# Optimization experiments

Hardware: AMD Instinct MI355X
Metric: run time of the kernel (lower is better)

Reference implementation:

```python
import jax, jax.numpy as jnp
import numpy as np

B, S, D, H = 2, 2048, 1024, 16
HD = D // H  # 64

def setup_inputs() -> dict:
    key = jax.random.key(0)
    ks = jax.random.split(key, 11)
    s = 1.0 / np.sqrt(D)
    inp = {
        "q": jax.random.normal(ks[0], (B, S, D), jnp.float32),
        "k": jax.random.normal(ks[1], (B, S, D), jnp.float32),
        "v": jax.random.normal(ks[2], (B, S, D), jnp.float32),
        "Wq": jax.random.normal(ks[3], (D, D), jnp.float32) * s,
        "bq": jnp.zeros((D,), jnp.float32),
        "Wk": jax.random.normal(ks[4], (D, D), jnp.float32) * s,
        "bk": jnp.zeros((D,), jnp.float32),
        "Wv": jax.random.normal(ks[5], (D, D), jnp.float32) * s,
        "bv": jnp.zeros((D,), jnp.float32),
        "Wo": jax.random.normal(ks[6], (D, D), jnp.float32) * s,
        "bo": jnp.zeros((D,), jnp.float32),
    }
    return inp

def _split_heads(x):
    # [B,S,D] -> [B,H,S,HD]
    b = x.shape[0]
    return x.reshape(b, -1, H, HD).transpose(0, 2, 1, 3)

def reference(q, k, v, Wq, bq, Wk, bk, Wv, bv, Wo, bo):
    qh = _split_heads(q @ Wq.T + bq)
    kh = _split_heads(k @ Wk.T + bk)
    vh = _split_heads(v @ Wv.T + bv)
    scale = 1.0 / jnp.sqrt(jnp.asarray(HD, qh.dtype))
    scores = jnp.einsum("bhqd,bhkd->bhqk", qh, kh) * scale  # [B,H,S,S]
    atten = jax.nn.softmax(scores, axis=-1)  # dropout is eval-mode no-op
    ctx = jnp.einsum("bhqk,bhkd->bhqd", atten, vh)
    out = ctx.transpose(0, 2, 1, 3).reshape(q.shape[0], -1, D)
    return out @ Wo.T + bo, atten
```

## Files before the change

kernel.cpp:

```cpp
#include <hip/hip_runtime.h>
#include <cstdint>

#define B_ 2
#define S_ 2048
#define D_ 1024
#define H_ 16

typedef __bf16 bf16x8 __attribute__((ext_vector_type(8)));
typedef float  f32x4  __attribute__((ext_vector_type(4)));

__device__ __forceinline__ void g2l16(const void* g, void* l) {
  auto* gp = reinterpret_cast<const __attribute__((address_space(1))) uint32_t*>(
      reinterpret_cast<uintptr_t>(g));
  auto* lp = reinterpret_cast<__attribute__((address_space(3))) uint32_t*>(
      reinterpret_cast<uintptr_t>(l));
  __builtin_amdgcn_global_load_lds(gp, lp, 16, 0, 0);
}

__device__ __forceinline__ float exp2_hw(float x) {
#if __has_builtin(__builtin_amdgcn_exp2f)
  return __builtin_amdgcn_exp2f(x);
#else
  return __exp2f(x);
#endif
}

struct CvtArgs {
  const float* s[7];
  __bf16* d[7];
  int n[7];
};

__global__ __launch_bounds__(256) void k_cvt(CvtArgs a) {
  int t = blockIdx.y;
  long i = (long)blockIdx.x * blockDim.x + threadIdx.x;
  long base = i * 8;
  if (base >= a.n[t]) return;
  const float4* sp = (const float4*)(a.s[t] + base);
  float4 x = sp[0], y = sp[1];
  bf16x8 o;
  o[0] = (__bf16)x.x; o[1] = (__bf16)x.y; o[2] = (__bf16)x.z; o[3] = (__bf16)x.w;
  o[4] = (__bf16)y.x; o[5] = (__bf16)y.y; o[6] = (__bf16)y.z; o[7] = (__bf16)y.w;
  *(bf16x8*)(a.d[t] + base) = o;
}

__global__ __launch_bounds__(256, 3) void k_proj(
    const __bf16* __restrict__ Xq, const __bf16* __restrict__ Xk, const __bf16* __restrict__ Xv,
    const __bf16* __restrict__ Wq, const __bf16* __restrict__ Wk, const __bf16* __restrict__ Wv,
    const float* __restrict__ bq, const float* __restrict__ bk, const float* __restrict__ bv,
    __bf16* __restrict__ Oq, __bf16* __restrict__ Ok, __bf16* __restrict__ Ov)
{
  int z = blockIdx.z;
  const __bf16* X = (z == 0) ? Xq : (z == 1) ? Xk : Xv;
  const __bf16* W = (z == 0) ? Wq : (z == 1) ? Wk : Wv;
  const float* bias = (z == 0) ? bq : (z == 1) ? bk : bv;
  __bf16* O = (z == 0) ? Oq : (z == 1) ? Ok : Ov;
  float scale = (z == 0) ? 0.180336880111183f : 1.0f;

  __shared__ bf16x8 As[2][512];
  __shared__ bf16x8 Bs[2][512];

  int t = threadIdx.x, lane = t & 63, w = t >> 6;
  int l15 = lane & 15, l4 = lane >> 4;
  int wr = w >> 1, wc = w & 1;
  int m0 = blockIdx.y * 128, n0 = blockIdx.x * 128;

  int srow = t >> 2, sc = t & 3;
  int ldsoff = __builtin_amdgcn_readfirstlane(w * 1024);
  const __bf16* Xs = X + (size_t)(m0 + srow) * 1024 + sc * 8;
  const __bf16* Wsp = W + (size_t)(n0 + srow) * 1024 + sc * 8;

#define PSTAGE(buf, kt)                                                        \
  {                                                                            \
    _Pragma("unroll")                                                          \
    for (int i = 0; i < 2; ++i) {                                              \
      int lo = __builtin_amdgcn_readfirstlane(i * 4096 + ldsoff);              \
      g2l16(Xs + (size_t)i * 64 * 1024 + (kt) * 32, (char*)As[buf] + lo);      \
      g2l16(Wsp + (size_t)i * 64 * 1024 + (kt) * 32, (char*)Bs[buf] + lo);     \
    }                                                                          \
  }

  f32x4 acc[4][4] = {};

  PSTAGE(0, 0)
  asm volatile("s_waitcnt vmcnt(0)" ::: "memory");
  __builtin_amdgcn_s_barrier();
  __builtin_amdgcn_sched_barrier(0);

  for (int kt = 0; kt < 32; ++kt) {
    int cur = kt & 1;
    if (kt < 31) PSTAGE(cur ^ 1, kt + 1)

    bf16x8 af[4], bfr[4];
#pragma unroll
    for (int i = 0; i < 4; ++i) af[i] = As[cur][(wr * 64 + i * 16 + l15) * 4 + l4];
#pragma unroll
    for (int j = 0; j < 4; ++j) bfr[j] = Bs[cur][(wc * 64 + j * 16 + l15) * 4 + l4];
#pragma unroll
    for (int i = 0; i < 4; ++i)
#pragma unroll
      for (int j = 0; j < 4; ++j)
        acc[i][j] = __builtin_amdgcn_mfma_f32_16x16x32_bf16(af[i], bfr[j], acc[i][j], 0, 0, 0);

    asm volatile("s_waitcnt vmcnt(0)" ::: "memory");
    __builtin_amdgcn_s_barrier();
    __builtin_amdgcn_sched_barrier(0);
  }
#undef PSTAGE

#pragma unroll
  for (int j = 0; j < 4; ++j) {
    int col = n0 + wc * 64 + j * 16 + l15;
    float bv_ = bias[col];
    int h = col >> 6, hd = col & 63;
#pragma unroll
    for (int i = 0; i < 4; ++i) {
#pragma unroll
      for (int r = 0; r < 4; ++r) {
        int row = m0 + wr * 64 + i * 16 + l4 * 4 + r;
        int b = row >> 11, ss = row & 2047;
        float val = (acc[i][j][r] + bv_) * scale;
        O[(((size_t)b * H_ + h) * S_ + ss) * 64 + hd] = (__bf16)val;
      }
    }
  }
}

__global__ __launch_bounds__(256) void k_trans(const __bf16* __restrict__ Vh,
                                               __bf16* __restrict__ VhT)
{
  __shared__ __bf16 Tt[64][72];
  int bid = blockIdx.x;
  int bh = bid >> 5, st = bid & 31;
  int t = threadIdx.x;
  int sr = t >> 2, dc = (t & 3) * 16;
  const __bf16* src = Vh + (((size_t)bh * S_) + st * 64 + sr) * 64 + dc;
  *(bf16x8*)&Tt[sr][dc] = *(const bf16x8*)src;
  *(bf16x8*)&Tt[sr][dc + 8] = *(const bf16x8*)(src + 8);
  __syncthreads();
  int dr = t >> 2, s0 = (t & 3) * 16;
  bf16x8 o0, o1;
#pragma unroll
  for (int ii = 0; ii < 8; ++ii) { o0[ii] = Tt[s0 + ii][dr]; o1[ii] = Tt[s0 + 8 + ii][dr]; }
  __bf16* dst = VhT + ((size_t)bh * 64 + dr) * S_ + st * 64 + s0;
  *(bf16x8*)dst = o0;
  *(bf16x8*)(dst + 8) = o1;
}

__global__ __launch_bounds__(512, 4) void k_attn(
    const __bf16* __restrict__ Qh, const __bf16* __restrict__ Kh,
    const __bf16* __restrict__ VhT, float* __restrict__ atten,
    __bf16* __restrict__ ctxb)
{
  __shared__ bf16x8 Kl[2][512];
  __shared__ bf16x8 Vl[2][512];
  __shared__ bf16x8 Pl[8 * 176];

  int bid = blockIdx.x;
  int sb = (bid & 7) * 64 + (bid >> 3);
  int bh = sb >> 4, qt = sb & 15;
  int t = threadIdx.x, lane = t & 63, w = t >> 6;
  int l15 = lane & 15, l4 = lane >> 4;
  int q0 = qt * 128 + w * 16;

  const __bf16* Qp = Qh + ((size_t)bh * S_ + q0) * 64;
  bf16x8 qf0 = *(const bf16x8*)(Qp + (size_t)l15 * 64 + l4 * 8);
  bf16x8 qf1 = *(const bf16x8*)(Qp + (size_t)l15 * 64 + 32 + l4 * 8);

  int srow = t >> 3, sc8 = t & 7;
  int scs = sc8 ^ (srow & 7);
  int ldsoff = __builtin_amdgcn_readfirstlane(w * 1024);

  const __bf16* KpS = Kh + (size_t)bh * S_ * 64 + (size_t)srow * 64 + scs * 8;
  const __bf16* VpS = VhT + (size_t)bh * 64 * S_ + (size_t)srow * S_ + scs * 8;

#define QK_TILES(KBUF, SC)                                                        \
  _Pragma("unroll")                                                               \
  for (int t8 = 0; t8 < 4; ++t8) {                                                \
    int kr = t8 * 16 + l15;                                                       \
    bf16x8 kf0 = (KBUF)[kr * 8 + ((l4) ^ (kr & 7))];                              \
    bf16x8 kf1 = (KBUF)[kr * 8 + ((4 + l4) ^ (kr & 7))];                          \
    f32x4 a_ = {0.f, 0.f, 0.f, 0.f};                                              \
    a_ = __builtin_amdgcn_mfma_f32_16x16x32_bf16(qf0, kf0, a_, 0, 0, 0);          \
    a_ = __builtin_amdgcn_mfma_f32_16x16x32_bf16(qf1, kf1, a_, 0, 0, 0);          \
    SC[t8] = a_;                                                                  \
  }

  float l_part[4] = {0.f, 0.f, 0.f, 0.f};

  g2l16(KpS, (char*)Kl[0] + ldsoff);
  asm volatile("s_waitcnt vmcnt(0)" ::: "memory");
  __builtin_amdgcn_s_barrier();
  __builtin_amdgcn_sched_barrier(0);

  for (int kt = 0; kt < 32; ++kt) {
    int cur = kt & 1;
    if (kt < 31) g2l16(KpS + (size_t)(kt + 1) * 4096, (char*)Kl[cur ^ 1] + ldsoff);
    __builtin_amdgcn_sched_barrier(0);

    f32x4 sc[4];
    QK_TILES(Kl[cur], sc)

#pragma unroll
    for (int r = 0; r < 4; ++r)
      l_part[r] += (exp2_hw(sc[0][r]) + exp2_hw(sc[1][r])) +
                   (exp2_hw(sc[2][r]) + exp2_hw(sc[3][r]));

    asm volatile("s_waitcnt vmcnt(0)" ::: "memory");
    __builtin_amdgcn_s_barrier();
    __builtin_amdgcn_sched_barrier(0);
  }

  float inv_l[4];
#pragma unroll
  for (int r = 0; r < 4; ++r) {
    float l = l_part[r];
    l += __shfl_xor(l, 1);
    l += __shfl_xor(l, 2);
    l += __shfl_xor(l, 4);
    l += __shfl_xor(l, 8);
    inv_l[r] = 1.0f / l;
  }

  f32x4 ctx[4] = {};
  float* aRow = atten + ((size_t)bh * S_ + q0) * S_;
  __bf16* PlW = (__bf16*)(Pl + w * 176);

  g2l16(KpS, (char*)Kl[0] + ldsoff);
  g2l16(VpS, (char*)Vl[0] + ldsoff);
  asm volatile("s_waitcnt vmcnt(0)" ::: "memory");
  __builtin_amdgcn_s_barrier();
  __builtin_amdgcn_sched_barrier(0);

  for (int kt = 0; kt < 32; ++kt) {
    int cur = kt & 1;
    if (kt < 31) {
      g2l16(KpS + (size_t)(kt + 1) * 4096, (char*)Kl[cur ^ 1] + ldsoff);
      g2l16(VpS + (size_t)(kt + 1) * 64, (char*)Vl[cur ^ 1] + ldsoff);
    }
    __builtin_amdgcn_sched_barrier(0);

    f32x4 sc[4];
    QK_TILES(Kl[cur], sc)

#pragma unroll
    for (int t8 = 0; t8 < 4; ++t8) {
#pragma unroll
      for (int r = 0; r < 4; ++r) {
        float p = exp2_hw(sc[t8][r]) * inv_l[r];
        aRow[(size_t)(l4 * 4 + r) * S_ + kt * 64 + t8 * 16 + l15] = p;
        PlW[(l4 * 4 + r) * 88 + t8 * 16 + l15] = (__bf16)p;
      }
    }

#pragma unroll
    for (int kc = 0; kc < 2; ++kc) {
      bf16x8 pa = Pl[w * 176 + l15 * 11 + kc * 4 + l4];
#pragma unroll
      for (int dt = 0; dt < 4; ++dt) {
        int vr = dt * 16 + l15;
        bf16x8 vf = Vl[cur][vr * 8 + ((kc * 4 + l4) ^ (vr & 7))];
        ctx[dt] = __builtin_amdgcn_mfma_f32_16x16x32_bf16(pa, vf, ctx[dt], 0, 0, 0);
      }
    }

    asm volatile("s_waitcnt vmcnt(16)" ::: "memory");
    __builtin_amdgcn_s_barrier();
    __builtin_amdgcn_sched_barrier(0);
  }

  int b = bh >> 4, h = bh & 15;
#pragma unroll
  for (int dt = 0; dt < 4; ++dt) {
#pragma unroll
    for (int r = 0; r < 4; ++r) {
      size_t row = (size_t)b * S_ + q0 + l4 * 4 + r;
      ctxb[row * D_ + h * 64 + dt * 16 + l15] = (__bf16)ctx[dt][r];
    }
  }
#undef QK_TILES
}

__global__ __launch_bounds__(256, 3) void k_out(
    const __bf16* __restrict__ X, const __bf16* __restrict__ W,
    const float* __restrict__ bias, float* __restrict__ O)
{
  __shared__ bf16x8 As[2][512];
  __shared__ bf16x8 Bs[2][512];

  int t = threadIdx.x, lane = t & 63, w = t >> 6;
  int l15 = lane & 15, l4 = lane >> 4;
  int wr = w >> 1, wc = w & 1;
  int m0 = blockIdx.y * 128, n0 = blockIdx.x * 128;

  int srow = t >> 2, sc = t & 3;
  int ldsoff = __builtin_amdgcn_readfirstlane(w * 1024);
  const __bf16* Xs = X + (size_t)(m0 + srow) * 1024 + sc * 8;
  const __bf16* Wsp = W + (size_t)(n0 + srow) * 1024 + sc * 8;

#define PSTAGE(buf, kt)                                                        \
  {                                                                            \
    _Pragma("unroll")                                                          \
    for (int i = 0; i < 2; ++i) {                                              \
      int lo = __builtin_amdgcn_readfirstlane(i * 4096 + ldsoff);              \
      g2l16(Xs + (size_t)i * 64 * 1024 + (kt) * 32, (char*)As[buf] + lo);      \
      g2l16(Wsp + (size_t)i * 64 * 1024 + (kt) * 32, (char*)Bs[buf] + lo);     \
    }                                                                          \
  }

  f32x4 acc[4][4] = {};

  PSTAGE(0, 0)
  asm volatile("s_waitcnt vmcnt(0)" ::: "memory");
  __builtin_amdgcn_s_barrier();
  __builtin_amdgcn_sched_barrier(0);

  for (int kt = 0; kt < 32; ++kt) {
    int cur = kt & 1;
    if (kt < 31) PSTAGE(cur ^ 1, kt + 1)

    bf16x8 af[4], bfr[4];
#pragma unroll
    for (int i = 0; i < 4; ++i) af[i] = As[cur][(wr * 64 + i * 16 + l15) * 4 + l4];
#pragma unroll
    for (int j = 0; j < 4; ++j) bfr[j] = Bs[cur][(wc * 64 + j * 16 + l15) * 4 + l4];
#pragma unroll
    for (int i = 0; i < 4; ++i)
#pragma unroll
      for (int j = 0; j < 4; ++j)
        acc[i][j] = __builtin_amdgcn_mfma_f32_16x16x32_bf16(af[i], bfr[j], acc[i][j], 0, 0, 0);

    asm volatile("s_waitcnt vmcnt(0)" ::: "memory");
    __builtin_amdgcn_s_barrier();
    __builtin_amdgcn_sched_barrier(0);
  }
#undef PSTAGE

#pragma unroll
  for (int j = 0; j < 4; ++j) {
    int col = n0 + wc * 64 + j * 16 + l15;
    float bv_ = bias[col];
#pragma unroll
    for (int i = 0; i < 4; ++i) {
#pragma unroll
      for (int r = 0; r < 4; ++r) {
        int row = m0 + wr * 64 + i * 16 + l4 * 4 + r;
        O[(size_t)row * 1024 + col] = acc[i][j][r] + bv_;
      }
    }
  }
}

extern "C" void kernel_launch(void* const* d_in, const int* in_sizes, int n_in,
                              void* d_out, int out_size, void* d_ws, size_t ws_size,
                              hipStream_t stream)
{
  const float* q  = (const float*)d_in[0];
  const float* k  = (const float*)d_in[1];
  const float* v  = (const float*)d_in[2];
  const float* Wq = (const float*)d_in[3];
  const float* bq = (const float*)d_in[4];
  const float* Wk = (const float*)d_in[5];
  const float* bk = (const float*)d_in[6];
  const float* Wv = (const float*)d_in[7];
  const float* bv = (const float*)d_in[8];
  const float* Wo = (const float*)d_in[9];
  const float* bo = (const float*)d_in[10];

  const size_t NBSD = (size_t)B_ * S_ * D_;
  const size_t NDD  = (size_t)D_ * D_;

  float* out = (float*)d_out;
  float* atten = out + NBSD;

  if (ws_size < 2 * (NBSD * 4 + NDD * 4 + NBSD * 4)) return;

  __bf16* ws = (__bf16*)d_ws;
  __bf16* qb  = ws;
  __bf16* kb  = ws + NBSD;
  __bf16* vb  = ws + 2 * NBSD;
  __bf16* Wqb = ws + 3 * NBSD;
  __bf16* Wkb = Wqb + NDD;
  __bf16* Wvb = Wkb + NDD;
  __bf16* Wob = Wvb + NDD;
  __bf16* Qh  = Wob + NDD;
  __bf16* Kh  = Qh + NBSD;
  __bf16* Vh  = Kh + NBSD;
  __bf16* VhT = Vh + NBSD;
  __bf16* ctxb = qb;

  CvtArgs ca;
  ca.s[0] = q;  ca.d[0] = qb;  ca.n[0] = (int)NBSD;
  ca.s[1] = k;  ca.d[1] = kb;  ca.n[1] = (int)NBSD;
  ca.s[2] = v;  ca.d[2] = vb;  ca.n[2] = (int)NBSD;
  ca.s[3] = Wq; ca.d[3] = Wqb; ca.n[3] = (int)NDD;
  ca.s[4] = Wk; ca.d[4] = Wkb; ca.n[4] = (int)NDD;
  ca.s[5] = Wv; ca.d[5] = Wvb; ca.n[5] = (int)NDD;
  ca.s[6] = Wo; ca.d[6] = Wob; ca.n[6] = (int)NDD;

  k_cvt<<<dim3(2048, 7), 256, 0, stream>>>(ca);
  k_proj<<<dim3(8, 32, 3), 256, 0, stream>>>(qb, kb, vb, Wqb, Wkb, Wvb,
                                             bq, bk, bv, Qh, Kh, Vh);
  k_trans<<<dim3(1024), 256, 0, stream>>>(Vh, VhT);
  k_attn<<<dim3(512), 512, 0, stream>>>(Qh, Kh, VhT, atten, ctxb);
  k_out<<<dim3(8, 32), 256, 0, stream>>>(ctxb, Wob, bo, out);
}
```

Baseline: 264.4 us.

## Triple-buffer LDS pipelines in projection, attention and output kernels

Switches the GEMM and attention kernels from double to triple-buffered LDS rings with prefetch distance two, so waits only drain older loads (partial vmcnt) rather than all of them. The attention first pass now loads 128 keys per stage and folds exp-sum into the QK loop, and the K/V buffers are merged into one ring. Attention probabilities and output writes use nontemporal stores to cut cache pollution. This adds LDS usage, which may lower occupancy, and the hand-tuned vmcnt counts must match the number of outstanding loads.

```diff
diff --git a/kernel.cpp b/kernel.cpp
--- a/kernel.cpp
+++ b/kernel.cpp
@@ -57,8 +57,8 @@
   __bf16* O = (z == 0) ? Oq : (z == 1) ? Ok : Ov;
   float scale = (z == 0) ? 0.180336880111183f : 1.0f;
 
-  __shared__ bf16x8 As[2][512];
-  __shared__ bf16x8 Bs[2][512];
+  __shared__ bf16x8 As[3][512];
+  __shared__ bf16x8 Bs[3][512];
 
   int t = threadIdx.x, lane = t & 63, w = t >> 6;
   int l15 = lane & 15, l4 = lane >> 4;
@@ -83,13 +83,17 @@
   f32x4 acc[4][4] = {};
 
   PSTAGE(0, 0)
-  asm volatile("s_waitcnt vmcnt(0)" ::: "memory");
+  PSTAGE(1, 1)
+  asm volatile("s_waitcnt vmcnt(4)" ::: "memory");
   __builtin_amdgcn_s_barrier();
   __builtin_amdgcn_sched_barrier(0);
 
+  int ring = 0;
   for (int kt = 0; kt < 32; ++kt) {
-    int cur = kt & 1;
-    if (kt < 31) PSTAGE(cur ^ 1, kt + 1)
+    int cur = ring;
+    int rp2 = (ring == 0) ? 2 : ring - 1;
+    if (kt + 2 < 32) PSTAGE(rp2, kt + 2)
+    __builtin_amdgcn_sched_barrier(0);
 
     bf16x8 af[4], bfr[4];
 #pragma unroll
@@ -102,9 +106,16 @@
       for (int j = 0; j < 4; ++j)
         acc[i][j] = __builtin_amdgcn_mfma_f32_16x16x32_bf16(af[i], bfr[j], acc[i][j], 0, 0, 0);
 
-    asm volatile("s_waitcnt vmcnt(0)" ::: "memory");
-    __builtin_amdgcn_s_barrier();
-    __builtin_amdgcn_sched_barrier(0);
+    if (kt < 30) {
+      asm volatile("s_waitcnt vmcnt(4)" ::: "memory");
+      __builtin_amdgcn_s_barrier();
+      __builtin_amdgcn_sched_barrier(0);
+    } else if (kt == 30) {
+      asm volatile("s_waitcnt vmcnt(0)" ::: "memory");
+      __builtin_amdgcn_s_barrier();
+      __builtin_amdgcn_sched_barrier(0);
+    }
+    ring = (ring == 2) ? 0 : ring + 1;
   }
 #undef PSTAGE
 
@@ -152,8 +163,7 @@
     const __bf16* __restrict__ VhT, float* __restrict__ atten,
     __bf16* __restrict__ ctxb)
 {
-  __shared__ bf16x8 Kl[2][512];
-  __shared__ bf16x8 Vl[2][512];
+  __shared__ bf16x8 KVl[3][1024];
   __shared__ bf16x8 Pl[8 * 176];
 
   int bid = blockIdx.x;
@@ -169,47 +179,58 @@
 
   int srow = t >> 3, sc8 = t & 7;
   int scs = sc8 ^ (srow & 7);
-  int ldsoff = __builtin_amdgcn_readfirstlane(w * 1024);
+  int wbase = __builtin_amdgcn_readfirstlane(w * 1024);
 
   const __bf16* KpS = Kh + (size_t)bh * S_ * 64 + (size_t)srow * 64 + scs * 8;
   const __bf16* VpS = VhT + (size_t)bh * 64 * S_ + (size_t)srow * S_ + scs * 8;
 
-#define QK_TILES(KBUF, SC)                                                        \
-  _Pragma("unroll")                                                               \
-  for (int t8 = 0; t8 < 4; ++t8) {                                                \
-    int kr = t8 * 16 + l15;                                                       \
-    bf16x8 kf0 = (KBUF)[kr * 8 + ((l4) ^ (kr & 7))];                              \
-    bf16x8 kf1 = (KBUF)[kr * 8 + ((4 + l4) ^ (kr & 7))];                          \
-    f32x4 a_ = {0.f, 0.f, 0.f, 0.f};                                              \
-    a_ = __builtin_amdgcn_mfma_f32_16x16x32_bf16(qf0, kf0, a_, 0, 0, 0);          \
-    a_ = __builtin_amdgcn_mfma_f32_16x16x32_bf16(qf1, kf1, a_, 0, 0, 0);          \
-    SC[t8] = a_;                                                                  \
-  }
-
   float l_part[4] = {0.f, 0.f, 0.f, 0.f};
 
-  g2l16(KpS, (char*)Kl[0] + ldsoff);
-  asm volatile("s_waitcnt vmcnt(0)" ::: "memory");
+#define ASTAGE(buf, kt)                                                        \
+  {                                                                            \
+    g2l16(KpS + (size_t)(kt) * 8192, (char*)KVl[buf] + wbase);                 \
+    g2l16(KpS + (size_t)(kt) * 8192 + 4096, (char*)KVl[buf] + 8192 + wbase);   \
+  }
+
+  ASTAGE(0, 0)
+  ASTAGE(1, 1)
+  asm volatile("s_waitcnt vmcnt(2)" ::: "memory");
   __builtin_amdgcn_s_barrier();
   __builtin_amdgcn_sched_barrier(0);
 
-  for (int kt = 0; kt < 32; ++kt) {
-    int cur = kt & 1;
-    if (kt < 31) g2l16(KpS + (size_t)(kt + 1) * 4096, (char*)Kl[cur ^ 1] + ldsoff);
-    __builtin_amdgcn_sched_barrier(0);
-
-    f32x4 sc[4];
-    QK_TILES(Kl[cur], sc)
-
-#pragma unroll
-    for (int r = 0; r < 4; ++r)
-      l_part[r] += (exp2_hw(sc[0][r]) + exp2_hw(sc[1][r])) +
-                   (exp2_hw(sc[2][r]) + exp2_hw(sc[3][r]));
-
-    asm volatile("s_waitcnt vmcnt(0)" ::: "memory");
-    __builtin_amdgcn_s_barrier();
-    __builtin_amdgcn_sched_barrier(0);
-  }
+  {
+    int ring = 0;
+    for (int kt = 0; kt < 16; ++kt) {
+      int cur = ring;
+      int rp2 = (ring == 0) ? 2 : ring - 1;
+      if (kt + 2 < 16) ASTAGE(rp2, kt + 2)
+      __builtin_amdgcn_sched_barrier(0);
+
+#pragma unroll
+      for (int t8 = 0; t8 < 8; ++t8) {
+        int kr = t8 * 16 + l15;
+        bf16x8 kf0 = KVl[cur][kr * 8 + ((l4) ^ (kr & 7))];
+        bf16x8 kf1 = KVl[cur][kr * 8 + ((4 + l4) ^ (kr & 7))];
+        f32x4 a_ = {0.f, 0.f, 0.f, 0.f};
+        a_ = __builtin_amdgcn_mfma_f32_16x16x32_bf16(qf0, kf0, a_, 0, 0, 0);
+        a_ = __builtin_amdgcn_mfma_f32_16x16x32_bf16(qf1, kf1, a_, 0, 0, 0);
+#pragma unroll
+        for (int r = 0; r < 4; ++r) l_part[r] += exp2_hw(a_[r]);
+      }
+
+      if (kt < 14) {
+        asm volatile("s_waitcnt vmcnt(2)" ::: "memory");
+        __builtin_amdgcn_s_barrier();
+        __builtin_amdgcn_sched_barrier(0);
+      } else if (kt == 14) {
+        asm volatile("s_waitcnt vmcnt(0)" ::: "memory");
+        __builtin_amdgcn_s_barrier();
+        __builtin_amdgcn_sched_barrier(0);
+      }
+      ring = (ring == 2) ? 0 : ring + 1;
+    }
+  }
+#undef ASTAGE
 
   float inv_l[4];
 #pragma unroll
@@ -222,52 +243,76 @@
     inv_l[r] = 1.0f / l;
   }
 
+  __builtin_amdgcn_s_barrier();
+  __builtin_amdgcn_sched_barrier(0);
+
   f32x4 ctx[4] = {};
   float* aRow = atten + ((size_t)bh * S_ + q0) * S_;
   __bf16* PlW = (__bf16*)(Pl + w * 176);
 
-  g2l16(KpS, (char*)Kl[0] + ldsoff);
-  g2l16(VpS, (char*)Vl[0] + ldsoff);
-  asm volatile("s_waitcnt vmcnt(0)" ::: "memory");
+#define BSTAGE(buf, kt)                                                        \
+  {                                                                            \
+    g2l16(KpS + (size_t)(kt) * 4096, (char*)KVl[buf] + wbase);                 \
+    g2l16(VpS + (size_t)(kt) * 64, (char*)KVl[buf] + 8192 + wbase);            \
+  }
+
+  BSTAGE(0, 0)
+  BSTAGE(1, 1)
+  asm volatile("s_waitcnt vmcnt(2)" ::: "memory");
   __builtin_amdgcn_s_barrier();
   __builtin_amdgcn_sched_barrier(0);
 
-  for (int kt = 0; kt < 32; ++kt) {
-    int cur = kt & 1;
-    if (kt < 31) {
-      g2l16(KpS + (size_t)(kt + 1) * 4096, (char*)Kl[cur ^ 1] + ldsoff);
-      g2l16(VpS + (size_t)(kt + 1) * 64, (char*)Vl[cur ^ 1] + ldsoff);
-    }
-    __builtin_amdgcn_sched_barrier(0);
-
-    f32x4 sc[4];
-    QK_TILES(Kl[cur], sc)
-
-#pragma unroll
-    for (int t8 = 0; t8 < 4; ++t8) {
-#pragma unroll
-      for (int r = 0; r < 4; ++r) {
-        float p = exp2_hw(sc[t8][r]) * inv_l[r];
-        aRow[(size_t)(l4 * 4 + r) * S_ + kt * 64 + t8 * 16 + l15] = p;
-        PlW[(l4 * 4 + r) * 88 + t8 * 16 + l15] = (__bf16)p;
-      }
-    }
-
-#pragma unroll
-    for (int kc = 0; kc < 2; ++kc) {
-      bf16x8 pa = Pl[w * 176 + l15 * 11 + kc * 4 + l4];
-#pragma unroll
-      for (int dt = 0; dt < 4; ++dt) {
-        int vr = dt * 16 + l15;
-        bf16x8 vf = Vl[cur][vr * 8 + ((kc * 4 + l4) ^ (vr & 7))];
-        ctx[dt] = __builtin_amdgcn_mfma_f32_16x16x32_bf16(pa, vf, ctx[dt], 0, 0, 0);
-      }
-    }
-
-    asm volatile("s_waitcnt vmcnt(16)" ::: "memory");
-    __builtin_amdgcn_s_barrier();
-    __builtin_amdgcn_sched_barrier(0);
-  }
+  {
+    int ring = 0;
+    for (int kt = 0; kt < 32; ++kt) {
+      int cur = ring;
+      int rp2 = (ring == 0) ? 2 : ring - 1;
+      if (kt + 2 < 32) BSTAGE(rp2, kt + 2)
+      __builtin_amdgcn_sched_barrier(0);
+
+      f32x4 sc[4];
+#pragma unroll
+      for (int t8 = 0; t8 < 4; ++t8) {
+        int kr = t8 * 16 + l15;
+        bf16x8 kf0 = KVl[cur][kr * 8 + ((l4) ^ (kr & 7))];
+        bf16x8 kf1 = KVl[cur][kr * 8 + ((4 + l4) ^ (kr & 7))];
+        f32x4 a_ = {0.f, 0.f, 0.f, 0.f};
+        a_ = __builtin_amdgcn_mfma_f32_16x16x32_bf16(qf0, kf0, a_, 0, 0, 0);
+        a_ = __builtin_amdgcn_mfma_f32_16x16x32_bf16(qf1, kf1, a_, 0, 0, 0);
+        sc[t8] = a_;
+      }
+
+#pragma unroll
+      for (int t8 = 0; t8 < 4; ++t8) {
+#pragma unroll
+        for (int r = 0; r < 4; ++r) {
+          float p = exp2_hw(sc[t8][r]) * inv_l[r];
+          __builtin_nontemporal_store(
+              p, &aRow[(size_t)(l4 * 4 + r) * S_ + kt * 64 + t8 * 16 + l15]);
+          PlW[(l4 * 4 + r) * 88 + t8 * 16 + l15] = (__bf16)p;
+        }
+      }
+
+#pragma unroll
+      for (int kc = 0; kc < 2; ++kc) {
+        bf16x8 pa = Pl[w * 176 + l15 * 11 + kc * 4 + l4];
+#pragma unroll
+        for (int dt = 0; dt < 4; ++dt) {
+          int vr = dt * 16 + l15;
+          bf16x8 vf = KVl[cur][512 + vr * 8 + ((kc * 4 + l4) ^ (vr & 7))];
+          ctx[dt] = __builtin_amdgcn_mfma_f32_16x16x32_bf16(pa, vf, ctx[dt], 0, 0, 0);
+        }
+      }
+
+      if (kt < 31) {
+        asm volatile("s_waitcnt vmcnt(18)" ::: "memory");
+        __builtin_amdgcn_s_barrier();
+        __builtin_amdgcn_sched_barrier(0);
+      }
+      ring = (ring == 2) ? 0 : ring + 1;
+    }
+  }
+#undef BSTAGE
 
   int b = bh >> 4, h = bh & 15;
 #pragma unroll
@@ -278,15 +323,14 @@
       ctxb[row * D_ + h * 64 + dt * 16 + l15] = (__bf16)ctx[dt][r];
     }
   }
-#undef QK_TILES
 }
 
 __global__ __launch_bounds__(256, 3) void k_out(
     const __bf16* __restrict__ X, const __bf16* __restrict__ W,
     const float* __restrict__ bias, float* __restrict__ O)
 {
-  __shared__ bf16x8 As[2][512];
-  __shared__ bf16x8 Bs[2][512];
+  __shared__ bf16x8 As[3][512];
+  __shared__ bf16x8 Bs[3][512];
 
   int t = threadIdx.x, lane = t & 63, w = t >> 6;
   int l15 = lane & 15, l4 = lane >> 4;
@@ -311,13 +355,17 @@
   f32x4 acc[4][4] = {};
 
   PSTAGE(0, 0)
-  asm volatile("s_waitcnt vmcnt(0)" ::: "memory");
+  PSTAGE(1, 1)
+  asm volatile("s_waitcnt vmcnt(4)" ::: "memory");
   __builtin_amdgcn_s_barrier();
   __builtin_amdgcn_sched_barrier(0);
 
+  int ring = 0;
   for (int kt = 0; kt < 32; ++kt) {
-    int cur = kt & 1;
-    if (kt < 31) PSTAGE(cur ^ 1, kt + 1)
+    int cur = ring;
+    int rp2 = (ring == 0) ? 2 : ring - 1;
+    if (kt + 2 < 32) PSTAGE(rp2, kt + 2)
+    __builtin_amdgcn_sched_barrier(0);
 
     bf16x8 af[4], bfr[4];
 #pragma unroll
@@ -330,9 +378,16 @@
       for (int j = 0; j < 4; ++j)
         acc[i][j] = __builtin_amdgcn_mfma_f32_16x16x32_bf16(af[i], bfr[j], acc[i][j], 0, 0, 0);
 
-    asm volatile("s_waitcnt vmcnt(0)" ::: "memory");
-    __builtin_amdgcn_s_barrier();
-    __builtin_amdgcn_sched_barrier(0);
+    if (kt < 30) {
+      asm volatile("s_waitcnt vmcnt(4)" ::: "memory");
+      __builtin_amdgcn_s_barrier();
+      __builtin_amdgcn_sched_barrier(0);
+    } else if (kt == 30) {
+      asm volatile("s_waitcnt vmcnt(0)" ::: "memory");
+      __builtin_amdgcn_s_barrier();
+      __builtin_amdgcn_sched_barrier(0);
+    }
+    ring = (ring == 2) ? 0 : ring + 1;
   }
 #undef PSTAGE
 
@@ -345,7 +400,7 @@
 #pragma unroll
       for (int r = 0; r < 4; ++r) {
         int row = m0 + wr * 64 + i * 16 + l4 * 4 + r;
-        O[(size_t)row * 1024 + col] = acc[i][j][r] + bv_;
+        __builtin_nontemporal_store(acc[i][j][r] + bv_, &O[(size_t)row * 1024 + col]);
       }
     }
   }
```

Measured after the change: 274.1 us. +3.6%, slower.
